# Kernel optimization log

Measured on AMD Instinct MI355X. Metric: run time of the kernel, lower is better.

The kernel has to match this reference:

```python
import jax, jax.numpy as jnp
import numpy as np

DIM = 512; NH = 8; HD = DIM // NH; WS = 28; N = WS * WS; H3 = (DIM * 4) // 3; EPS = 1e-6; B = 16


def _rel_pos_index(H, W):
    # static numpy computation of Swin-style relative position index [N, N]
    coords = np.stack(np.meshgrid(np.arange(H), np.arange(W), indexing='ij')).reshape(2, -1)
    rel = (coords[:, :, None] - coords[:, None, :]).transpose(1, 2, 0)
    rel[..., 0] += H - 1
    rel[..., 1] += W - 1
    rel[..., 0] *= 2 * W - 1
    return rel.sum(-1)

RPI = jnp.asarray(_rel_pos_index(WS, WS))  # [N, N] int


def adaptive_ln(x, w, b, a1w, a1b, a2w, a2b):
    # x: [B,C,H,W]; adapt params from global-avg-pooled 1x1 convs (== matmuls)
    C = x.shape[1]
    pooled = x.mean(axis=(2, 3))                      # [B,C]
    h = jax.nn.relu(pooled @ a1w.T + a1b)             # [B,C/4]
    ad = h @ a2w.T + a2b                              # [B,2C]
    aw = ad[:, :C][:, :, None, None]
    ab = ad[:, C:][:, :, None, None]
    u = x.mean(axis=1, keepdims=True)
    s = ((x - u) ** 2).mean(axis=1, keepdims=True)
    xn = (x - u) * jax.lax.rsqrt(s + EPS)
    return (w[None, :, None, None] * (1.0 + aw)) * xn + (b[None, :, None, None] + ab)


def dwconv(x, w, b):
    y = jax.lax.conv_general_dilated(x, w, (1, 1), 'SAME', feature_group_count=x.shape[1],
                                     dimension_numbers=('NCHW', 'OIHW', 'NCHW'))
    return y + b[None, :, None, None]


def conv1x1(x, w, b):
    return jnp.einsum('bchw,oc->bohw', x, w) + b[None, :, None, None]


def _forward(x, face_priors, n1_w, n1_b, n1_a1w, n1_a1b, n1_a2w, n1_a2b,
             n2_w, n2_b, n2_a1w, n2_a1b, n2_a2w, n2_a2b,
             qkv_w, qkv_b, rpb_table, struct_prior, proj_w, proj_b,
             eye_w, eye_b, nose_w, nose_b, mouth_w, mouth_b,
             fusion_w, fusion_b, gate1_w, gate1_b, gate2_w, gate2_b,
             es1_w, es1_b, es2_w, es2_b, em1_w, em1_b, em2_w, em2_b,
             el1_w, el1_b, el2_w, el2_b, router_w, router_b):
    Bx, C, H, W = x.shape
    n = H * W
    shortcut = x
    xa = adaptive_ln(x, n1_w, n1_b, n1_a1w, n1_a1b, n1_a2w, n1_a2b)
    # --- TripletFaceAttention ---
    xf = xa.reshape(Bx, C, n).transpose(0, 2, 1)                     # [B,N,C]
    qkv = (xf @ qkv_w.T + qkv_b).reshape(Bx, n, 3, NH, HD).transpose(2, 0, 3, 1, 4)
    q, k, v = qkv[0], qkv[1], qkv[2]                                 # [B,h,N,d]
    attn = jnp.einsum('bhnd,bhmd->bhnm', q, k) * (HD ** -0.5)
    attn = attn + struct_prior                                       # learned structure prior [1,h,N,N]
    rpb = rpb_table[RPI]                                             # [N,N,h]
    attn = attn + jnp.transpose(rpb, (2, 0, 1))[None]                # + relative position bias
    attn = attn * face_priors[:, None]                               # multiplicative face mask
    attn = jax.nn.softmax(attn, axis=-1)
    o = jnp.einsum('bhnm,bhmd->bhnd', attn, v).transpose(0, 2, 1, 3).reshape(Bx, n, C)
    o = o @ proj_w.T + proj_b
    x = shortcut + o.transpose(0, 2, 1).reshape(Bx, C, H, W)
    # --- FaceTokenMixer ---
    xn2 = adaptive_ln(x, n2_w, n2_b, n2_a1w, n2_a1b, n2_a2w, n2_a2b)
    cat = jnp.concatenate([dwconv(xn2, eye_w, eye_b),
                           dwconv(xn2, nose_w, nose_b),
                           dwconv(xn2, mouth_w, mouth_b)], axis=1)   # [B,3C,H,W]
    g = jax.nn.sigmoid(conv1x1(jax.nn.relu(conv1x1(xn2, gate1_w, gate1_b)), gate2_w, gate2_b))
    x = x + conv1x1(cat * g, fusion_w, fusion_b)
    # --- EfficientMLP (3-expert MoE, soft routing) ---
    r = jax.nn.softmax(x.mean(axis=(2, 3)) @ router_w.T + router_b, axis=-1)  # [B,3]
    def expert(w1, b1, w2, b2):
        return conv1x1(jax.nn.gelu(conv1x1(x, w1, b1), approximate=False), w2, b2)
    out = (r[:, 0, None, None, None] * expert(es1_w, es1_b, es2_w, es2_b)
           + r[:, 1, None, None, None] * expert(em1_w, em1_b, em2_w, em2_b)
           + r[:, 2, None, None, None] * expert(el1_w, el1_b, el2_w, el2_b))
    return x + out


def setup_inputs() -> dict:
    ks = iter(jax.random.split(jax.random.key(0), 64))
    def rn(shape, s=0.02):
        return jax.random.normal(next(ks), shape, jnp.float32) * s
    d = {}
    d['x'] = jax.random.normal(next(ks), (B, DIM, WS, WS), jnp.float32)
    d['face_priors'] = jax.random.uniform(next(ks), (B, N, N), jnp.float32)
    for p in ('n1', 'n2'):
        d[p + '_w'] = jnp.ones((DIM,), jnp.float32)
        d[p + '_b'] = jnp.zeros((DIM,), jnp.float32)
        d[p + '_a1w'] = rn((DIM // 4, DIM)); d[p + '_a1b'] = jnp.zeros((DIM // 4,), jnp.float32)
        d[p + '_a2w'] = rn((2 * DIM, DIM // 4)); d[p + '_a2b'] = jnp.zeros((2 * DIM,), jnp.float32)
    d['qkv_w'] = rn((3 * DIM, DIM)); d['qkv_b'] = jnp.zeros((3 * DIM,), jnp.float32)
    d['rpb_table'] = rn(((2 * WS - 1) ** 2, NH))
    d['struct_prior'] = rn((1, NH, N, N))
    d['proj_w'] = rn((DIM, DIM)); d['proj_b'] = jnp.zeros((DIM,), jnp.float32)
    d['eye_w'] = rn((DIM, 1, 3, 3)); d['eye_b'] = jnp.zeros((DIM,), jnp.float32)
    d['nose_w'] = rn((DIM, 1, 5, 5)); d['nose_b'] = jnp.zeros((DIM,), jnp.float32)
    d['mouth_w'] = rn((DIM, 1, 7, 7)); d['mouth_b'] = jnp.zeros((DIM,), jnp.float32)
    d['fusion_w'] = rn((DIM, 3 * DIM)); d['fusion_b'] = jnp.zeros((DIM,), jnp.float32)
    d['gate1_w'] = rn((DIM // 4, DIM)); d['gate1_b'] = jnp.zeros((DIM // 4,), jnp.float32)
    d['gate2_w'] = rn((3 * DIM, DIM // 4)); d['gate2_b'] = jnp.zeros((3 * DIM,), jnp.float32)
    for e in ('es', 'em', 'el'):
        d[e + '1_w'] = rn((H3, DIM)); d[e + '1_b'] = jnp.zeros((H3,), jnp.float32)
        d[e + '2_w'] = rn((DIM, H3)); d[e + '2_b'] = jnp.zeros((DIM,), jnp.float32)
    d['router_w'] = rn((3, DIM)); d['router_b'] = jnp.zeros((3,), jnp.float32)
    return d


def reference(x, face_priors, n1_w, n1_b, n1_a1w, n1_a1b, n1_a2w, n1_a2b,
              n2_w, n2_b, n2_a1w, n2_a1b, n2_a2w, n2_a2b,
              qkv_w, qkv_b, rpb_table, struct_prior, proj_w, proj_b,
              eye_w, eye_b, nose_w, nose_b, mouth_w, mouth_b,
              fusion_w, fusion_b, gate1_w, gate1_b, gate2_w, gate2_b,
              es1_w, es1_b, es2_w, es2_b, em1_w, em1_b, em2_w, em2_b,
              el1_w, el1_b, el2_w, el2_b, router_w, router_b):
    return _forward(x, face_priors, n1_w, n1_b, n1_a1w, n1_a1b, n1_a2w, n1_a2b,
                    n2_w, n2_b, n2_a1w, n2_a1b, n2_a2w, n2_a2b,
                    qkv_w, qkv_b, rpb_table, struct_prior, proj_w, proj_b,
                    eye_w, eye_b, nose_w, nose_b, mouth_w, mouth_b,
                    fusion_w, fusion_b, gate1_w, gate1_b, gate2_w, gate2_b,
                    es1_w, es1_b, es2_w, es2_b, em1_w, em1_b, em2_w, em2_b,
                    el1_w, el1_b, el2_w, el2_b, router_w, router_b)
```

## Files before the change

### kernel.cpp

```cpp
#include <hip/hip_runtime.h>
#include <math.h>


#define NPIX 784
#define CDIM 512
#define NHEAD 8
#define C3 1536

typedef unsigned int uint;
typedef unsigned short ushort;
typedef float f32x4 __attribute__((ext_vector_type(4)));
typedef __bf16 bf16x8 __attribute__((ext_vector_type(8)));
typedef __bf16 bf16x2 __attribute__((ext_vector_type(2)));

#define LOG2E 1.4426950408889634f
#define KSCL  0.18033688011112042f

#define OFF_XPM ((size_t)0)
#define OFF_W   ((size_t)3211264)
#define OFF_R2  ((size_t)5324288)
#define OFF_VBF ((size_t)14958080)
#define OFF_OBF ((size_t)18169344)
#define OFF_X2  ((size_t)21380608)
#define OFF_X3  ((size_t)27803136)
#define OFF_PL  ((size_t)34225664)
#define OFF_AD  ((size_t)34233856)
#define OFF_RB  ((size_t)34250240)
#define OFF_US  ((size_t)34250288)
#define OFF_RS  ((size_t)34262832)
#define OFF_E2C ((size_t)34275392)

#define WOFF_QKV 0
#define WOFF_PROJ 786432
#define WOFF_G1  1048576
#define WOFF_G2  1114112
#define WOFF_FUS 1310720
#define WOFF_E1  2097152

__device__ __forceinline__ ushort f2bf(float f) {
  __bf16 h = (__bf16)f;
  return __builtin_bit_cast(ushort, h);
}
__device__ __forceinline__ unsigned pack2bf(float lo, float hi) {
  bf16x2 v = {(__bf16)lo, (__bf16)hi};
  return __builtin_bit_cast(unsigned, v);
}
__device__ __forceinline__ float bf2f(ushort u) {
  unsigned x = ((unsigned)u) << 16;
  return __builtin_bit_cast(float, x);
}
__device__ __forceinline__ void unpack4bf(uint2 v, float* o) {
  o[0] = bf2f((ushort)(v.x & 0xffffu)); o[1] = bf2f((ushort)(v.x >> 16));
  o[2] = bf2f((ushort)(v.y & 0xffffu)); o[3] = bf2f((ushort)(v.y >> 16));
}

__global__ __launch_bounds__(64) void pool_mean_k(const float* __restrict__ x,
                                                  float* __restrict__ pooled) {
  int c = blockIdx.x, b = blockIdx.y;
  const float* row = x + ((size_t)b * CDIM + c) * NPIX;
  float s = 0.f;
  for (int i = threadIdx.x; i < NPIX; i += 64) s += row[i];
  #pragma unroll
  for (int off = 32; off; off >>= 1) s += __shfl_down(s, off);
  if (threadIdx.x == 0) pooled[b * CDIM + c] = s;
}

__global__ __launch_bounds__(256) void adapt_mlp_k(const float* __restrict__ pooled,
                                                   const float* __restrict__ a1w,
                                                   const float* __restrict__ a1b,
                                                   const float* __restrict__ a2w,
                                                   const float* __restrict__ a2b,
                                                   float* __restrict__ ad) {
  int b = blockIdx.x, tid = threadIdx.x;
  __shared__ float pl[CDIM];
  __shared__ float hh[128];
  for (int i = tid; i < CDIM; i += 256)
    pl[i] = pooled[b * CDIM + i] * (1.f / NPIX);
  __syncthreads();
  if (tid < 128) {
    const float* w = a1w + (size_t)tid * CDIM;
    float a = a1b[tid];
    for (int k = 0; k < CDIM; ++k) a += w[k] * pl[k];
    hh[tid] = fmaxf(a, 0.f);
  }
  __syncthreads();
  for (int o = tid; o < 1024; o += 256) {
    const float* w = a2w + (size_t)o * 128;
    float a = a2b[o];
    for (int k = 0; k < 128; ++k) a += w[k] * hh[k];
    ad[b * 1024 + o] = a;
  }
}

template <int STATS>
__global__ __launch_bounds__(256) void ln_pm_k(const float* __restrict__ x,
                                               const float* __restrict__ w,
                                               const float* __restrict__ bias,
                                               const float* __restrict__ ad,
                                               ushort* __restrict__ out,
                                               float* __restrict__ ust,
                                               float* __restrict__ rstp) {
  int b = blockIdx.y;
  int p0 = blockIdx.x * 32;
  int tid = threadIdx.x;
  int px = tid & 31, cg = tid >> 5;
  int p = p0 + px;
  bool valid = p < NPIX;
  const float* xb = x + (size_t)b * CDIM * NPIX;
  float s = 0.f, s2 = 0.f;
  if (valid) {
    for (int c = cg * 64; c < cg * 64 + 64; ++c) {
      float v = xb[(size_t)c * NPIX + p];
      s += v; s2 += v * v;
    }
  }
  __shared__ float rs[8][32], rq[8][32], us[32], vs[32];
  rs[cg][px] = s; rq[cg][px] = s2;
  __syncthreads();
  if (tid < 32) {
    float ts = 0.f, ts2 = 0.f;
    #pragma unroll
    for (int g = 0; g < 8; ++g) { ts += rs[g][tid]; ts2 += rq[g][tid]; }
    float u = ts * (1.f / CDIM);
    float var = ts2 * (1.f / CDIM) - u * u;
    float rv = rsqrtf(var + 1e-6f);
    us[tid] = u; vs[tid] = rv;
    if (STATS && p0 + tid < NPIX) {
      ust[(size_t)b * NPIX + p0 + tid] = u;
      rstp[(size_t)b * NPIX + p0 + tid] = rv;
    }
  }
  __syncthreads();
  if (valid) {
    float u = us[px], rv = vs[px];
    const float* aw = ad + (size_t)b * 1024;
    const float* ab = aw + CDIM;
    ushort* ob = out + ((size_t)(b * NPIX + p)) * CDIM + cg * 64;
    for (int cb = 0; cb < 64; cb += 8) {
      int c = cg * 64 + cb;
      float vv[8];
      #pragma unroll
      for (int q = 0; q < 8; ++q) {
        float v = xb[(size_t)(c + q) * NPIX + p];
        vv[q] = w[c + q] * (1.f + aw[c + q]) * ((v - u) * rv) + (bias[c + q] + ab[c + q]);
      }
      uint4 o = {pack2bf(vv[0], vv[1]), pack2bf(vv[2], vv[3]),
                 pack2bf(vv[4], vv[5]), pack2bf(vv[6], vv[7])};
      *(uint4*)(ob + cb) = o;
    }
  }
}

struct CvtDesc {
  const float* s[11];
  ushort* d[11];
  int rows[11], sk[11], dk[11], ds[11], rr[11];
};
__global__ __launch_bounds__(256) void cvt_w_k(CvtDesc D) {
  int seg = blockIdx.y;
  int sk = D.sk[seg], dk = D.dk[seg], ds = D.ds[seg], rr = D.rr[seg];
  int total = D.rows[seg] * dk;
  const float* s = D.s[seg];
  ushort* d = D.d[seg];
  for (int i = blockIdx.x * 256 + threadIdx.x; i < total; i += gridDim.x * 256) {
    int r = i / dk, cc = i - r * dk;
    d[(size_t)r * ds + cc] = (cc < sk && r < rr) ? f2bf(s[(size_t)r * sk + cc]) : (ushort)0;
  }
}

__global__ __launch_bounds__(256) void sprpb_k(const float* __restrict__ sp,
                                               const float* __restrict__ rpb,
                                               ushort* __restrict__ out) {
  const int q = blockIdx.x, h = blockIdx.y;
  const int i1 = q / 28, j1 = q - i1 * 28;
  const float* src = sp + ((size_t)h * NPIX + q) * NPIX;
  ushort* dst = out + ((size_t)h * NPIX + q) * NPIX;
  for (int m = threadIdx.x; m < NPIX; m += 256) {
    int i2 = m / 28, j2 = m - i2 * 28;
    float rv = rpb[(size_t)((i1 - i2 + 27) * 55 + (j1 - j2 + 27)) * NHEAD + h];
    dst[m] = f2bf((src[m] + rv) * LOG2E);
  }
}

__global__ __launch_bounds__(256) void fpcvt_k(const float* __restrict__ fp,
                                               ushort* __restrict__ out) {
  size_t i = (size_t)blockIdx.x * 256 + threadIdx.x;
  float4 v = *((const float4*)fp + i);
  ushort4 o;
  o.x = f2bf(v.x); o.y = f2bf(v.y); o.z = f2bf(v.z); o.w = f2bf(v.w);
  *((ushort4*)out + i) = o;
}

__global__ __launch_bounds__(512) void biaseff_k(const float* __restrict__ rbuf,
                                                 const float* __restrict__ b0,
                                                 const float* __restrict__ b1,
                                                 const float* __restrict__ b2,
                                                 const float* __restrict__ a0,
                                                 const float* __restrict__ a1,
                                                 const float* __restrict__ a2,
                                                 float* __restrict__ be,
                                                 float* __restrict__ e1bcat) {
  int b = blockIdx.x;
  if (b < 16) {
    int n = threadIdx.x;
    be[b * 512 + n] = rbuf[b * 3] * b0[n] + rbuf[b * 3 + 1] * b1[n] + rbuf[b * 3 + 2] * b2[n];
  } else {
    for (int i = threadIdx.x; i < 2112; i += 512) {
      int e = i / 704, r = i - e * 704;
      e1bcat[i] = (r < 682) ? (e == 0 ? a0 : e == 1 ? a1 : a2)[r] : 0.f;
    }
  }
}

template <int ORIENT, int EPI, int POOL, int DUALBF, int BN>
__global__ __launch_bounds__(256) void mgemm_k(const ushort* __restrict__ X,
                                               const ushort* __restrict__ Wt,
                                               const float* __restrict__ bias,
                                               const float* __restrict__ resid,
                                               const float* __restrict__ scales,
                                               void* __restrict__ OutV,
                                               float* __restrict__ pool_out,
                                               ushort* __restrict__ pm_out,
                                               int Ks, int Nreal, int Nstore) {
  constexpr int NFRAG = BN / 64;
  const int bid = blockIdx.x;
  const int xcd = bid & 7;
  const int i = bid >> 3;
  const int mt_local = i % 14;
  const int nt = i / 14;
  const int m0 = (xcd * 14 + mt_local) * 112;
  const int n0 = nt * BN;
  const int bb = m0 / NPIX;
  const int t = threadIdx.x;
  const int w = t >> 6, lane = t & 63, c = lane & 15, g = lane >> 4;
  __shared__ ushort Xs[7168];
  __shared__ ushort Ws[BN * 64];
  f32x4 acc[7][NFRAG];
  #pragma unroll
  for (int mi = 0; mi < 7; ++mi)
    #pragma unroll
    for (int ni = 0; ni < NFRAG; ++ni) acc[mi][ni] = (f32x4){0.f, 0.f, 0.f, 0.f};

  for (int k0 = 0; k0 < Ks; k0 += 64) {
    for (int ii = t; ii < 896; ii += 256) {
      int m = ii >> 3, kg = ii & 7;
      uint4 v = *(const uint4*)(X + (size_t)(m0 + m) * Ks + k0 + kg * 8);
      *(uint4*)&Xs[m * 64 + ((kg ^ (m & 7)) << 3)] = v;
    }
    for (int ii = t; ii < BN * 8; ii += 256) {
      int n = ii >> 3, kg = ii & 7;
      uint4 v = {0u, 0u, 0u, 0u};
      if (n0 + n < Nreal) v = *(const uint4*)(Wt + (size_t)(n0 + n) * Ks + k0 + kg * 8);
      *(uint4*)&Ws[n * 64 + ((kg ^ (n & 7)) << 3)] = v;
    }
    __syncthreads();
    #pragma unroll
    for (int kc = 0; kc < 2; ++kc) {
      bf16x8 xf[7], wf[NFRAG];
      #pragma unroll
      for (int mi = 0; mi < 7; ++mi) {
        int m = mi * 16 + c;
        xf[mi] = *(const bf16x8*)&Xs[m * 64 + (((kc * 4 + g) ^ (m & 7)) << 3)];
      }
      #pragma unroll
      for (int ni = 0; ni < NFRAG; ++ni) {
        int n = w * (16 * NFRAG) + ni * 16 + c;
        wf[ni] = *(const bf16x8*)&Ws[n * 64 + (((kc * 4 + g) ^ (n & 7)) << 3)];
      }
      #pragma unroll
      for (int mi = 0; mi < 7; ++mi)
        #pragma unroll
        for (int ni = 0; ni < NFRAG; ++ni)
          acc[mi][ni] = (ORIENT == 0)
            ? __builtin_amdgcn_mfma_f32_16x16x32_bf16(wf[ni], xf[mi], acc[mi][ni], 0, 0, 0)
            : __builtin_amdgcn_mfma_f32_16x16x32_bf16(xf[mi], wf[ni], acc[mi][ni], 0, 0, 0);
    }
    __syncthreads();
  }

  if (ORIENT == 0) {
    ushort* Ob = (ushort*)OutV;
    const int nbq = n0 + w * (16 * NFRAG);
    float bi[NFRAG][4];
    #pragma unroll
    for (int ni = 0; ni < NFRAG; ++ni)
      #pragma unroll
      for (int j = 0; j < 4; ++j) {
        int n = nbq + ni * 16 + g * 4 + j;
        bi[ni][j] = (n < Nreal) ? bias[n] : 0.f;
      }
    #pragma unroll
    for (int mi = 0; mi < 7; ++mi) {
      int m = m0 + mi * 16 + c;
      #pragma unroll
      for (int ni = 0; ni < NFRAG; ++ni) {
        int nb = nbq + ni * 16 + g * 4;
        if (nb >= Nstore) continue;
        float v[4];
        #pragma unroll
        for (int j = 0; j < 4; ++j) v[j] = acc[mi][ni][j] + bi[ni][j];
        if (EPI == 1) {
          #pragma unroll
          for (int j = 0; j < 4; ++j) v[j] = fmaxf(v[j], 0.f);
        } else if (EPI == 2) {
          #pragma unroll
          for (int j = 0; j < 4; ++j)
            v[j] = 0.5f * v[j] * (1.f + erff(v[j] * 0.70710678118654752f));
        } else if (EPI == 3) {
          uint2 cm = *(const uint2*)&Ob[(size_t)m * Nstore + nb];
          float cf[4];
          unpack4bf(cm, cf);
          #pragma unroll
          for (int j = 0; j < 4; ++j)
            v[j] = (1.f / (1.f + __expf(-v[j]))) * cf[j];
        } else if (EPI == 5) {
          int e = nb / 704; e = (e > 2) ? 2 : e;
          float sc = scales[bb * 3 + e];
          #pragma unroll
          for (int j = 0; j < 4; ++j)
            v[j] = 0.5f * v[j] * (1.f + erff(v[j] * 0.70710678118654752f)) * sc;
        }
        uint2 o = {pack2bf(v[0], v[1]), pack2bf(v[2], v[3])};
        *(uint2*)&Ob[(size_t)m * Nstore + nb] = o;
      }
    }
  } else {
    const int prow = m0 - bb * NPIX;
    float* Ob = (float*)OutV + (size_t)bb * CDIM * NPIX;
    const float* Rb = resid + (size_t)bb * CDIM * NPIX;
    float sc = (EPI == 4 && scales) ? scales[bb * 3] : 1.f;
    #pragma unroll
    for (int ni = 0; ni < NFRAG; ++ni) {
      int n = n0 + w * (16 * NFRAG) + ni * 16 + c;
      float bv = (EPI == 5) ? bias[(size_t)bb * CDIM + n] : bias[n];
      float cs = 0.f;
      #pragma unroll
      for (int mi = 0; mi < 7; ++mi) {
        int p = prow + mi * 16 + g * 4;
        size_t off = (size_t)n * NPIX + p;
        float4 r = *(const float4*)&Rb[off];
        f32x4 a = acc[mi][ni];
        float4 o = {r.x + sc * (a[0] + bv), r.y + sc * (a[1] + bv),
                    r.z + sc * (a[2] + bv), r.w + sc * (a[3] + bv)};
        *(float4*)&Ob[off] = o;
        if (POOL) cs += o.x + o.y + o.z + o.w;
        if (DUALBF) {
          size_t mg = (size_t)(m0 + mi * 16 + g * 4);
          pm_out[mg * CDIM + n] = f2bf(o.x);
          pm_out[(mg + 1) * CDIM + n] = f2bf(o.y);
          pm_out[(mg + 2) * CDIM + n] = f2bf(o.z);
          pm_out[(mg + 3) * CDIM + n] = f2bf(o.w);
        }
      }
      if (POOL) {
        cs += __shfl_xor(cs, 16);
        cs += __shfl_xor(cs, 32);
        if (g == 0) atomicAdd(pool_out + (size_t)bb * CDIM + n, cs);
      }
    }
  }
}

__global__ __launch_bounds__(256) void vtr_k(const ushort* __restrict__ qkvbf,
                                             ushort* __restrict__ vbf) {
  const int p0 = blockIdx.x * 64, c0 = blockIdx.y * 64, b = blockIdx.z;
  __shared__ ushort T[64][72];
  for (int idx = threadIdx.x; idx < 512; idx += 256) {
    int pl = idx >> 3, cq = idx & 7;
    int p = p0 + pl;
    uint4 v = {0u, 0u, 0u, 0u};
    if (p < NPIX)
      v = *(const uint4*)(qkvbf + (size_t)(b * NPIX + p) * C3 + 1024 + c0 + cq * 8);
    *(uint4*)&T[pl][cq * 8] = v;
  }
  __syncthreads();
  for (int idx = threadIdx.x; idx < 512; idx += 256) {
    int cl = idx >> 3, pq = idx & 7;
    if (p0 + pq * 8 < NPIX) {
      ushort tmp[8];
      #pragma unroll
      for (int i = 0; i < 8; ++i) tmp[i] = T[pq * 8 + i][cl];
      *(uint4*)(vbf + ((size_t)(b * CDIM + c0 + cl)) * NPIX + p0 + pq * 8) =
          *(const uint4*)&tmp[0];
    }
  }
}

struct KFr { bf16x8 a0, a1, b0, b1; };
struct VFr { bf16x8 v0, v1, v2, v3; };
struct BFr { uint2 sl, fl, sh, fh; };

__global__ __launch_bounds__(256) void attn_mfma_k(const ushort* __restrict__ qkvbf,
                                                   const ushort* __restrict__ vbf,
                                                   const ushort* __restrict__ sprpb,
                                                   const ushort* __restrict__ fpb,
                                                   ushort* __restrict__ obf) {
  const int bid = blockIdx.x;
  const int xcd = bid & 7;
  const int i = bid >> 3;
  const int b = xcd + 8 * (i / 56);
  const int r = i % 56;
  const int h = r & 7;
  const int qt = r >> 3;
  const int w = threadIdx.x >> 6, lane = threadIdx.x & 63;
  const int g = lane >> 4, c = lane & 15;
  const int q0 = qt * 128 + w * 32;
  if (q0 >= NPIX) return;
  const bool hasB = (q0 + 16) < NPIX;
  const int qA = q0 + c;
  const int qB = q0 + 16 + c;

  __shared__ uint BL[4][2][384];
  uint* bwA = BL[w][0];
  uint* bwB = BL[w][1];

  const ushort* qpA = qkvbf + (size_t)(b * NPIX + qA) * C3 + h * 64 + g * 8;
  const bf16x8 qfA0 = *(const bf16x8*)qpA;
  const bf16x8 qfA1 = *(const bf16x8*)(qpA + 32);
  bf16x8 qfB0 = qfA0, qfB1 = qfA1;
  if (hasB) {
    const ushort* qpB = qkvbf + (size_t)(b * NPIX + qB) * C3 + h * 64 + g * 8;
    qfB0 = *(const bf16x8*)qpB;
    qfB1 = *(const bf16x8*)(qpB + 32);
  }

  const ushort* kbase = qkvbf + (size_t)b * NPIX * C3 + 512 + h * 64 + g * 8;
  const ushort* vbase = vbf + ((size_t)b * CDIM + h * 64) * NPIX;
  const ushort* sprA = sprpb + ((size_t)h * NPIX + qA) * NPIX;
  const ushort* sprB = sprpb + ((size_t)h * NPIX + (hasB ? qB : qA)) * NPIX;
  const ushort* fpA = fpb + ((size_t)b * NPIX + qA) * NPIX;
  const ushort* fpB = fpb + ((size_t)b * NPIX + (hasB ? qB : qA)) * NPIX;

  auto load_k = [&](int m0, bool tfull) -> KFr {
    KFr k;
    const ushort* kp = kbase + (size_t)(m0 + c) * C3;
    k.a0 = *(const bf16x8*)kp;
    k.a1 = *(const bf16x8*)(kp + 32);
    const ushort* kp1 = kp + (tfull ? (size_t)16 * C3 : 0);
    k.b0 = *(const bf16x8*)kp1;
    k.b1 = *(const bf16x8*)(kp1 + 32);
    return k;
  };
  auto load_v = [&](int m0) -> VFr {
    VFr v;
    const ushort* vp = vbase + (size_t)c * NPIX + m0 + g * 8;
    v.v0 = *(const bf16x8*)(vp);
    v.v1 = *(const bf16x8*)(vp + (size_t)16 * NPIX);
    v.v2 = *(const bf16x8*)(vp + (size_t)32 * NPIX);
    v.v3 = *(const bf16x8*)(vp + (size_t)48 * NPIX);
    return v;
  };
  auto load_b = [&](const ushort* spr, const ushort* fp, int m0) -> BFr {
    BFr x;
    x.sl = *(const uint2*)(spr + m0 + g * 4);
    x.fl = *(const uint2*)(fp + m0 + g * 4);
    x.sh = *(const uint2*)(spr + m0 + 16 + g * 4);
    x.fh = *(const uint2*)(fp + m0 + 16 + g * 4);
    return x;
  };

  f32x4 oA0 = {0.f, 0.f, 0.f, 0.f}, oA1 = oA0, oA2 = oA0, oA3 = oA0;
  f32x4 oB0 = oA0, oB1 = oA0, oB2 = oA0, oB3 = oA0;
  float MA = -1e30f, LA = 0.f, MB = -1e30f, LB = 0.f;

  KFr kc = load_k(0, true);
  VFr vc = load_v(0);
  BFr bcA = load_b(sprA, fpA, 0);
  BFr bcB = bcA;
  if (hasB) bcB = load_b(sprB, fpB, 0);

  for (int ms = 0; ms < 25; ++ms) {
    const int m0 = ms * 32;
    const bool full = (ms < 24);

    KFr kn; VFr vn; BFr bnA, bnB;
    if (full) {
      const int nm0 = m0 + 32;
      kn = load_k(nm0, ms + 1 < 24);
      vn = load_v(nm0);
      bnA = load_b(sprA, fpA, nm0);
      if (hasB) bnB = load_b(sprB, fpB, nm0);
    }

    f32x4 sA0 = {0.f, 0.f, 0.f, 0.f}, sA1 = sA0;
    __builtin_amdgcn_s_setprio(1);
    sA0 = __builtin_amdgcn_mfma_f32_16x16x32_bf16(kc.a0, qfA0, sA0, 0, 0, 0);
    sA0 = __builtin_amdgcn_mfma_f32_16x16x32_bf16(kc.a1, qfA1, sA0, 0, 0, 0);
    if (full) {
      sA1 = __builtin_amdgcn_mfma_f32_16x16x32_bf16(kc.b0, qfA0, sA1, 0, 0, 0);
      sA1 = __builtin_amdgcn_mfma_f32_16x16x32_bf16(kc.b1, qfA1, sA1, 0, 0, 0);
    }
    __builtin_amdgcn_s_setprio(0);
    {
      float vA0[4], vA1[4];
      float spv[4], fpv[4];
      unpack4bf(bcA.sl, spv);
      unpack4bf(bcA.fl, fpv);
      #pragma unroll
      for (int j = 0; j < 4; ++j) vA0[j] = fmaf(sA0[j], KSCL, spv[j]) * fpv[j];
      if (full) {
        unpack4bf(bcA.sh, spv);
        unpack4bf(bcA.fh, fpv);
        #pragma unroll
        for (int j = 0; j < 4; ++j) vA1[j] = fmaf(sA1[j], KSCL, spv[j]) * fpv[j];
      }
      float tm = fmaxf(fmaxf(vA0[0], vA0[1]), fmaxf(vA0[2], vA0[3]));
      if (full) tm = fmaxf(tm, fmaxf(fmaxf(vA1[0], vA1[1]), fmaxf(vA1[2], vA1[3])));
      tm = fmaxf(tm, __shfl_xor(tm, 16));
      tm = fmaxf(tm, __shfl_xor(tm, 32));
      if (__any(tm > MA)) {
        const float nM = fmaxf(MA, tm);
        const float fac = __builtin_amdgcn_exp2f(MA - nM);
        LA *= fac;
        #pragma unroll
        for (int j = 0; j < 4; ++j) { oA0[j] *= fac; oA1[j] *= fac; oA2[j] *= fac; oA3[j] *= fac; }
        MA = nM;
      }
      float p0v[4], p1v[4];
      float ps = 0.f;
      #pragma unroll
      for (int j = 0; j < 4; ++j) { p0v[j] = __builtin_amdgcn_exp2f(vA0[j] - MA); ps += p0v[j]; }
      if (full) {
        #pragma unroll
        for (int j = 0; j < 4; ++j) { p1v[j] = __builtin_amdgcn_exp2f(vA1[j] - MA); ps += p1v[j]; }
      }
      ps += __shfl_xor(ps, 16);
      ps += __shfl_xor(ps, 32);
      LA += ps;
      uint2 wlo, whi;
      wlo.x = pack2bf(p0v[0], p0v[1]);
      wlo.y = pack2bf(p0v[2], p0v[3]);
      whi.x = full ? pack2bf(p1v[0], p1v[1]) : 0u;
      whi.y = full ? pack2bf(p1v[2], p1v[3]) : 0u;
      *(uint2*)&bwA[lane * 6] = wlo;
      *(uint2*)&bwA[lane * 6 + 2] = whi;
    }

    if (hasB) {
      f32x4 sB0 = {0.f, 0.f, 0.f, 0.f}, sB1 = sB0;
      __builtin_amdgcn_s_setprio(1);
      sB0 = __builtin_amdgcn_mfma_f32_16x16x32_bf16(kc.a0, qfB0, sB0, 0, 0, 0);
      sB0 = __builtin_amdgcn_mfma_f32_16x16x32_bf16(kc.a1, qfB1, sB0, 0, 0, 0);
      if (full) {
        sB1 = __builtin_amdgcn_mfma_f32_16x16x32_bf16(kc.b0, qfB0, sB1, 0, 0, 0);
        sB1 = __builtin_amdgcn_mfma_f32_16x16x32_bf16(kc.b1, qfB1, sB1, 0, 0, 0);
      }
      __builtin_amdgcn_s_setprio(0);
      float vB0[4], vB1[4];
      float spv[4], fpv[4];
      unpack4bf(bcB.sl, spv);
      unpack4bf(bcB.fl, fpv);
      #pragma unroll
      for (int j = 0; j < 4; ++j) vB0[j] = fmaf(sB0[j], KSCL, spv[j]) * fpv[j];
      if (full) {
        unpack4bf(bcB.sh, spv);
        unpack4bf(bcB.fh, fpv);
        #pragma unroll
        for (int j = 0; j < 4; ++j) vB1[j] = fmaf(sB1[j], KSCL, spv[j]) * fpv[j];
      }
      float tm = fmaxf(fmaxf(vB0[0], vB0[1]), fmaxf(vB0[2], vB0[3]));
      if (full) tm = fmaxf(tm, fmaxf(fmaxf(vB1[0], vB1[1]), fmaxf(vB1[2], vB1[3])));
      tm = fmaxf(tm, __shfl_xor(tm, 16));
      tm = fmaxf(tm, __shfl_xor(tm, 32));
      if (__any(tm > MB)) {
        const float nM = fmaxf(MB, tm);
        const float fac = __builtin_amdgcn_exp2f(MB - nM);
        LB *= fac;
        #pragma unroll
        for (int j = 0; j < 4; ++j) { oB0[j] *= fac; oB1[j] *= fac; oB2[j] *= fac; oB3[j] *= fac; }
        MB = nM;
      }
      float p0v[4], p1v[4];
      float ps = 0.f;
      #pragma unroll
      for (int j = 0; j < 4; ++j) { p0v[j] = __builtin_amdgcn_exp2f(vB0[j] - MB); ps += p0v[j]; }
      if (full) {
        #pragma unroll
        for (int j = 0; j < 4; ++j) { p1v[j] = __builtin_amdgcn_exp2f(vB1[j] - MB); ps += p1v[j]; }
      }
      ps += __shfl_xor(ps, 16);
      ps += __shfl_xor(ps, 32);
      LB += ps;
      uint2 wlo, whi;
      wlo.x = pack2bf(p0v[0], p0v[1]);
      wlo.y = pack2bf(p0v[2], p0v[3]);
      whi.x = full ? pack2bf(p1v[0], p1v[1]) : 0u;
      whi.y = full ? pack2bf(p1v[2], p1v[3]) : 0u;
      *(uint2*)&bwB[lane * 6] = wlo;
      *(uint2*)&bwB[lane * 6 + 2] = whi;
    }

    const int f = g >> 1;
    const int slo = 32 * (g & 1) + c;
    uint2 blo = *(const uint2*)&bwA[slo * 6 + f * 2];
    uint2 bhi = *(const uint2*)&bwA[(slo + 16) * 6 + f * 2];
    uint4 bba = {blo.x, blo.y, bhi.x, bhi.y};
    const bf16x8 pfA = __builtin_bit_cast(bf16x8, bba);
    __builtin_amdgcn_s_setprio(1);
    oA0 = __builtin_amdgcn_mfma_f32_16x16x32_bf16(vc.v0, pfA, oA0, 0, 0, 0);
    oA1 = __builtin_amdgcn_mfma_f32_16x16x32_bf16(vc.v1, pfA, oA1, 0, 0, 0);
    oA2 = __builtin_amdgcn_mfma_f32_16x16x32_bf16(vc.v2, pfA, oA2, 0, 0, 0);
    oA3 = __builtin_amdgcn_mfma_f32_16x16x32_bf16(vc.v3, pfA, oA3, 0, 0, 0);
    __builtin_amdgcn_s_setprio(0);
    if (hasB) {
      uint2 clo = *(const uint2*)&bwB[slo * 6 + f * 2];
      uint2 chi = *(const uint2*)&bwB[(slo + 16) * 6 + f * 2];
      uint4 bbb = {clo.x, clo.y, chi.x, chi.y};
      const bf16x8 pfB = __builtin_bit_cast(bf16x8, bbb);
      __builtin_amdgcn_s_setprio(1);
      oB0 = __builtin_amdgcn_mfma_f32_16x16x32_bf16(vc.v0, pfB, oB0, 0, 0, 0);
      oB1 = __builtin_amdgcn_mfma_f32_16x16x32_bf16(vc.v1, pfB, oB1, 0, 0, 0);
      oB2 = __builtin_amdgcn_mfma_f32_16x16x32_bf16(vc.v2, pfB, oB2, 0, 0, 0);
      oB3 = __builtin_amdgcn_mfma_f32_16x16x32_bf16(vc.v3, pfB, oB3, 0, 0, 0);
      __builtin_amdgcn_s_setprio(0);
    }

    if (full) { kc = kn; vc = vn; bcA = bnA; if (hasB) bcB = bnB; }
  }

  {
    const float invL = 1.f / LA;
    ushort* dst = obf + (size_t)(b * NPIX + qA) * CDIM + h * 64 + g * 4;
    f32x4 ot[4] = {oA0, oA1, oA2, oA3};
    #pragma unroll
    for (int t2 = 0; t2 < 4; ++t2) {
      uint2 o = {pack2bf(ot[t2][0] * invL, ot[t2][1] * invL),
                 pack2bf(ot[t2][2] * invL, ot[t2][3] * invL)};
      *(uint2*)(dst + t2 * 16) = o;
    }
  }
  if (hasB) {
    const float invL = 1.f / LB;
    ushort* dst = obf + (size_t)(b * NPIX + qB) * CDIM + h * 64 + g * 4;
    f32x4 ot[4] = {oB0, oB1, oB2, oB3};
    #pragma unroll
    for (int t2 = 0; t2 < 4; ++t2) {
      uint2 o = {pack2bf(ot[t2][0] * invL, ot[t2][1] * invL),
                 pack2bf(ot[t2][2] * invL, ot[t2][3] * invL)};
      *(uint2*)(dst + t2 * 16) = o;
    }
  }
}

__device__ __forceinline__ float bf2f_s(ushort u) { return bf2f(u); }

template <int R>
__device__ __forceinline__ void conv_pass(const ushort* __restrict__ plane_ci,
                                          const float* __restrict__ wl_ci,
                                          float bv, int slot,
                                          ushort (*__restrict__ outb)[16], int ci) {
  constexpr int K = 2 * R + 1;
  float wreg[K * K];
  #pragma unroll
  for (int i = 0; i < K * K; ++i) wreg[i] = wl_ci[i];
  #pragma unroll
  for (int r7 = 0; r7 < 7; ++r7) {
    const int run = slot + r7 * 16;
    const int y = run >> 2, x0 = (run & 3) * 7;
    float acc[7];
    #pragma unroll
    for (int i = 0; i < 7; ++i) acc[i] = bv;
    #pragma unroll
    for (int dy = 0; dy < K; ++dy) {
      const ushort* rp = plane_ci + (y + 3 - R + dy) * 34 + (x0 + 3 - R);
      float win[7 + 2 * R];
      #pragma unroll
      for (int k = 0; k < 7 + 2 * R; ++k) win[k] = bf2f_s(rp[k]);
      #pragma unroll
      for (int i = 0; i < 7; ++i)
        #pragma unroll
        for (int k = 0; k < K; ++k)
          acc[i] = fmaf(win[i + k], wreg[dy * K + k], acc[i]);
    }
    #pragma unroll
    for (int i = 0; i < 7; ++i) outb[y * 28 + x0 + i][ci] = f2bf(acc[i]);
  }
}

__global__ __launch_bounds__(256) void dwln_k(const float* __restrict__ x2,
    const float* __restrict__ ust, const float* __restrict__ rst,
    const float* __restrict__ ad, const float* __restrict__ n2w,
    const float* __restrict__ n2b,
    const float* __restrict__ ew, const float* __restrict__ eb,
    const float* __restrict__ nw, const float* __restrict__ nb,
    const float* __restrict__ mw, const float* __restrict__ mb,
    ushort* __restrict__ cat) {
  const int cg = blockIdx.x, b = blockIdx.y;
  const int c0 = cg * 16;
  const int t = threadIdx.x;
  const int ci = t & 15, slot = t >> 4;

  __shared__ ushort plane[16][1156];
  __shared__ ushort outb[784][16];
  __shared__ float Wl[16 * 49];
  __shared__ float LWs[16], LBs[16];

  {
    uint* pz = (uint*)&plane[0][0];
    for (int i = t; i < 16 * 1156 / 2; i += 256) pz[i] = 0u;
  }
  if (t < 16) {
    int cc = c0 + t;
    float aw = ad[b * 1024 + cc], ab = ad[b * 1024 + 512 + cc];
    LWs[t] = n2w[cc] * (1.f + aw);
    LBs[t] = n2b[cc] + ab;
  }
  __syncthreads();

  {
    float uu[4], rr[4];
    #pragma unroll
    for (int j = 0; j < 4; ++j) {
      int p = t + j * 256;
      if (p < NPIX) {
        uu[j] = ust[(size_t)b * NPIX + p];
        rr[j] = rst[(size_t)b * NPIX + p];
      }
    }
    for (int cc = 0; cc < 16; ++cc) {
      const float* xp = x2 + ((size_t)(b * CDIM + c0 + cc)) * NPIX;
      float lw = LWs[cc], lb = LBs[cc];
      #pragma unroll
      for (int j = 0; j < 4; ++j) {
        int p = t + j * 256;
        if (p < NPIX) {
          int y = p / 28, xx2 = p - y * 28;
          plane[cc][(y + 3) * 34 + xx2 + 3] = f2bf(lw * (xp[p] - uu[j]) * rr[j] + lb);
        }
      }
    }
  }
  __syncthreads();

  #pragma unroll 1
  for (int cv = 0; cv < 3; ++cv) {
    const float* gw = (cv == 0) ? ew : (cv == 1) ? nw : mw;
    const float* gb = (cv == 0) ? eb : (cv == 1) ? nb : mb;
    const int K2 = (cv == 0) ? 9 : (cv == 1) ? 25 : 49;
    for (int i = t; i < 16 * K2; i += 256) {
      int cc = i / K2, k = i - cc * K2;
      Wl[cc * K2 + k] = gw[(size_t)(c0 + cc) * K2 + k];
    }
    __syncthreads();
    float bv = gb[c0 + ci];
    if (cv == 0)      conv_pass<1>(&plane[ci][0], &Wl[ci * 9],  bv, slot, outb, ci);
    else if (cv == 1) conv_pass<2>(&plane[ci][0], &Wl[ci * 25], bv, slot, outb, ci);
    else              conv_pass<3>(&plane[ci][0], &Wl[ci * 49], bv, slot, outb, ci);
    __syncthreads();
    for (int idx = t; idx < NPIX * 2; idx += 256) {
      int p = idx >> 1, half = idx & 1;
      uint4 v = *(const uint4*)&outb[p][half * 8];
      *(uint4*)(cat + ((size_t)(b * NPIX + p)) * C3 + cv * 512 + c0 + half * 8) = v;
    }
    __syncthreads();
  }
}

__global__ __launch_bounds__(64) void router_k(const float* __restrict__ pooled,
                                               const float* __restrict__ rw,
                                               const float* __restrict__ rb,
                                               float* __restrict__ r) {
  int b = blockIdx.x, lane = threadIdx.x;
  float a0 = 0.f, a1 = 0.f, a2 = 0.f;
  for (int k = lane; k < CDIM; k += 64) {
    float p = pooled[b * CDIM + k] * (1.f / NPIX);
    a0 += rw[k] * p;
    a1 += rw[CDIM + k] * p;
    a2 += rw[2 * CDIM + k] * p;
  }
  #pragma unroll
  for (int off = 32; off; off >>= 1) {
    a0 += __shfl_down(a0, off);
    a1 += __shfl_down(a1, off);
    a2 += __shfl_down(a2, off);
  }
  if (lane == 0) {
    float l0 = a0 + rb[0], l1 = a1 + rb[1], l2 = a2 + rb[2];
    float mx = fmaxf(l0, fmaxf(l1, l2));
    float e0 = __expf(l0 - mx), e1 = __expf(l1 - mx), e2 = __expf(l2 - mx);
    float inv = 1.f / (e0 + e1 + e2);
    r[b * 3 + 0] = e0 * inv;
    r[b * 3 + 1] = e1 * inv;
    r[b * 3 + 2] = e2 * inv;
  }
}

extern "C" void kernel_launch(void* const* d_in, const int* in_sizes, int n_in,
                              void* d_out, int out_size, void* d_ws, size_t ws_size,
                              hipStream_t stream) {
  (void)in_sizes; (void)n_in; (void)out_size; (void)ws_size;
  const float* x         = (const float*)d_in[0];
  const float* fpri      = (const float*)d_in[1];
  const float* n1_w      = (const float*)d_in[2];
  const float* n1_b      = (const float*)d_in[3];
  const float* n1_a1w    = (const float*)d_in[4];
  const float* n1_a1b    = (const float*)d_in[5];
  const float* n1_a2w    = (const float*)d_in[6];
  const float* n1_a2b    = (const float*)d_in[7];
  const float* n2_w      = (const float*)d_in[8];
  const float* n2_b      = (const float*)d_in[9];
  const float* n2_a1w    = (const float*)d_in[10];
  const float* n2_a1b    = (const float*)d_in[11];
  const float* n2_a2w    = (const float*)d_in[12];
  const float* n2_a2b    = (const float*)d_in[13];
  const float* qkv_w     = (const float*)d_in[14];
  const float* qkv_b     = (const float*)d_in[15];
  const float* rpb_table = (const float*)d_in[16];
  const float* sprior    = (const float*)d_in[17];
  const float* proj_w    = (const float*)d_in[18];
  const float* proj_b    = (const float*)d_in[19];
  const float* eye_w     = (const float*)d_in[20];
  const float* eye_b     = (const float*)d_in[21];
  const float* nose_w    = (const float*)d_in[22];
  const float* nose_b    = (const float*)d_in[23];
  const float* mouth_w   = (const float*)d_in[24];
  const float* mouth_b   = (const float*)d_in[25];
  const float* fusion_w  = (const float*)d_in[26];
  const float* fusion_b  = (const float*)d_in[27];
  const float* gate1_w   = (const float*)d_in[28];
  const float* gate1_b   = (const float*)d_in[29];
  const float* gate2_w   = (const float*)d_in[30];
  const float* gate2_b   = (const float*)d_in[31];
  const float* e1w[3] = {(const float*)d_in[32], (const float*)d_in[36], (const float*)d_in[40]};
  const float* e1b[3] = {(const float*)d_in[33], (const float*)d_in[37], (const float*)d_in[41]};
  const float* e2w[3] = {(const float*)d_in[34], (const float*)d_in[38], (const float*)d_in[42]};
  const float* e2b[3] = {(const float*)d_in[35], (const float*)d_in[39], (const float*)d_in[43]};
  const float* router_w  = (const float*)d_in[44];
  const float* router_b  = (const float*)d_in[45];

  float* ws    = (float*)d_ws;
  ushort* xpm  = (ushort*)(ws + OFF_XPM);
  ushort* wb   = (ushort*)(ws + OFF_W);
  ushort* r2u  = (ushort*)(ws + OFF_R2);
  ushort* vbf  = (ushort*)(ws + OFF_VBF);
  ushort* obf  = (ushort*)(ws + OFF_OBF);
  float* x2    = ws + OFF_X2;
  float* x3    = ws + OFF_X3;
  float* pld   = ws + OFF_PL;
  float* adb   = ws + OFF_AD;
  float* rbuf  = ws + OFF_RB;
  float* ust   = ws + OFF_US;
  float* rst   = ws + OFF_RS;
  float* outp  = (float*)d_out;

  ushort* qkvw  = wb + WOFF_QKV;
  ushort* projw = wb + WOFF_PROJ;
  ushort* g1w   = wb + WOFF_G1;
  ushort* g2w   = wb + WOFF_G2;
  ushort* fusw  = wb + WOFF_FUS;
  ushort* e1cat = wb + WOFF_E1;
  ushort* e2cat = (ushort*)(ws + OFF_E2C);
  float* be     = adb;
  float* e1bcat = adb + 8192;

  ushort* fpbf   = (ushort*)x2;
  ushort* sprpbf = (ushort*)x3;

  CvtDesc D;
  auto seg = [&](int s2, const float* src, ushort* dst, int rows, int sk, int dk,
                 int ds, int rr) {
    D.s[s2] = src; D.d[s2] = dst; D.rows[s2] = rows; D.sk[s2] = sk;
    D.dk[s2] = dk; D.ds[s2] = ds; D.rr[s2] = rr;
  };
  seg(0, qkv_w,    qkvw,  1536, 512,  512,  512,  1536);
  seg(1, proj_w,   projw, 512,  512,  512,  512,  512);
  seg(2, gate1_w,  g1w,   128,  512,  512,  512,  128);
  seg(3, gate2_w,  g2w,   1536, 128,  128,  128,  1536);
  seg(4, fusion_w, fusw,  512,  1536, 1536, 1536, 512);
  for (int e = 0; e < 3; ++e) {
    seg(5 + e, e1w[e], e1cat + (size_t)e * 704 * 512, 704, 512, 512, 512, 682);
    seg(8 + e, e2w[e], e2cat + (size_t)e * 704,       512, 682, 704, 2112, 512);
  }
  cvt_w_k<<<dim3(512, 11), 256, 0, stream>>>(D);

  sprpb_k<<<dim3(NPIX, NHEAD), 256, 0, stream>>>(sprior, rpb_table, sprpbf);
  fpcvt_k<<<9604, 256, 0, stream>>>(fpri, fpbf);

  pool_mean_k<<<dim3(CDIM, 16), 64, 0, stream>>>(x, pld);
  adapt_mlp_k<<<16, 256, 0, stream>>>(pld, n1_a1w, n1_a1b, n1_a2w, n1_a2b, adb);
  ln_pm_k<0><<<dim3(25, 16), 256, 0, stream>>>(x, n1_w, n1_b, adb, xpm, nullptr, nullptr);

  mgemm_k<0, 0, 0, 0, 128><<<1344, 256, 0, stream>>>(xpm, qkvw, qkv_b, nullptr, nullptr,
                                                     r2u, nullptr, nullptr, 512, 1536, 1536);
  vtr_k<<<dim3(13, 8, 16), 256, 0, stream>>>(r2u, vbf);
  attn_mfma_k<<<896, 256, 0, stream>>>(r2u, vbf, sprpbf, fpbf, obf);
  hipMemsetAsync(pld, 0, 16 * CDIM * sizeof(float), stream);
  mgemm_k<1, 4, 1, 0, 64><<<896, 256, 0, stream>>>(obf, projw, proj_b, x, nullptr,
                                                   x2, pld, nullptr, 512, 512, 512);

  adapt_mlp_k<<<16, 256, 0, stream>>>(pld, n2_a1w, n2_a1b, n2_a2w, n2_a2b, adb);
  ln_pm_k<1><<<dim3(25, 16), 256, 0, stream>>>(x2, n2_w, n2_b, adb, xpm, ust, rst);
  dwln_k<<<dim3(32, 16), 256, 0, stream>>>(x2, ust, rst, adb, n2_w, n2_b,
                                           eye_w, eye_b, nose_w, nose_b, mouth_w, mouth_b,
                                           r2u);
  mgemm_k<0, 1, 0, 0, 64><<<224, 256, 0, stream>>>(xpm, g1w, gate1_b, nullptr, nullptr,
                                                   obf, nullptr, nullptr, 512, 128, 128);
  mgemm_k<0, 3, 0, 0, 128><<<1344, 256, 0, stream>>>(obf, g2w, gate2_b, nullptr, nullptr,
                                                     r2u, nullptr, nullptr, 128, 1536, 1536);
  hipMemsetAsync(pld, 0, 16 * CDIM * sizeof(float), stream);
  mgemm_k<1, 4, 1, 1, 64><<<896, 256, 0, stream>>>(r2u, fusw, fusion_b, x2, nullptr,
                                                   x3, pld, xpm, 1536, 512, 512);

  router_k<<<16, 64, 0, stream>>>(pld, router_w, router_b, rbuf);
  biaseff_k<<<17, 512, 0, stream>>>(rbuf, e2b[0], e2b[1], e2b[2],
                                    e1b[0], e1b[1], e1b[2], be, e1bcat);
  mgemm_k<0, 5, 0, 0, 128><<<1904, 256, 0, stream>>>(xpm, e1cat, e1bcat, nullptr, rbuf,
                                                     r2u, nullptr, nullptr, 512, 2112, 2112);
  mgemm_k<1, 5, 0, 0, 64><<<896, 256, 0, stream>>>(r2u, e2cat, be, x3, nullptr,
                                                   outp, nullptr, nullptr, 2112, 512, 512);
}
```

Measured before the change: 724.7 us.

## Fuse V transpose into QKV GEMM epilogue and deepen bias prefetch in attention

```diff
diff --git a/kernel.cpp b/kernel.cpp
--- a/kernel.cpp
+++ b/kernel.cpp
@@ -212,7 +212,7 @@
   }
 }
 
-template <int ORIENT, int EPI, int POOL, int DUALBF, int BN>
+template <int ORIENT, int EPI, int POOL, int DUALBF, int DUALV, int BN>
 __global__ __launch_bounds__(256) void mgemm_k(const ushort* __restrict__ X,
                                                const ushort* __restrict__ Wt,
                                                const float* __restrict__ bias,
@@ -322,6 +322,12 @@
         }
         uint2 o = {pack2bf(v[0], v[1]), pack2bf(v[2], v[3])};
         *(uint2*)&Ob[(size_t)m * Nstore + nb] = o;
+        if (DUALV && nb >= 1024) {
+          const int p = m - bb * NPIX;
+          #pragma unroll
+          for (int j = 0; j < 4; ++j)
+            pm_out[((size_t)bb * CDIM + (nb + j - 1024)) * NPIX + p] = f2bf(v[j]);
+        }
       }
     }
   } else {
@@ -357,31 +363,6 @@
         cs += __shfl_xor(cs, 32);
         if (g == 0) atomicAdd(pool_out + (size_t)bb * CDIM + n, cs);
       }
-    }
-  }
-}
-
-__global__ __launch_bounds__(256) void vtr_k(const ushort* __restrict__ qkvbf,
-                                             ushort* __restrict__ vbf) {
-  const int p0 = blockIdx.x * 64, c0 = blockIdx.y * 64, b = blockIdx.z;
-  __shared__ ushort T[64][72];
-  for (int idx = threadIdx.x; idx < 512; idx += 256) {
-    int pl = idx >> 3, cq = idx & 7;
-    int p = p0 + pl;
-    uint4 v = {0u, 0u, 0u, 0u};
-    if (p < NPIX)
-      v = *(const uint4*)(qkvbf + (size_t)(b * NPIX + p) * C3 + 1024 + c0 + cq * 8);
-    *(uint4*)&T[pl][cq * 8] = v;
-  }
-  __syncthreads();
-  for (int idx = threadIdx.x; idx < 512; idx += 256) {
-    int cl = idx >> 3, pq = idx & 7;
-    if (p0 + pq * 8 < NPIX) {
-      ushort tmp[8];
-      #pragma unroll
-      for (int i = 0; i < 8; ++i) tmp[i] = T[pq * 8 + i][cl];
-      *(uint4*)(vbf + ((size_t)(b * CDIM + c0 + cl)) * NPIX + p0 + pq * 8) =
-          *(const uint4*)&tmp[0];
     }
   }
 }
@@ -466,20 +447,29 @@
   KFr kc = load_k(0, true);
   VFr vc = load_v(0);
   BFr bcA = load_b(sprA, fpA, 0);
-  BFr bcB = bcA;
-  if (hasB) bcB = load_b(sprB, fpB, 0);
+  BFr bnA = load_b(sprA, fpA, 32);
+  BFr bcB = bcA, bnB = bnA;
+  if (hasB) {
+    bcB = load_b(sprB, fpB, 0);
+    bnB = load_b(sprB, fpB, 32);
+  }
 
   for (int ms = 0; ms < 25; ++ms) {
     const int m0 = ms * 32;
     const bool full = (ms < 24);
 
-    KFr kn; VFr vn; BFr bnA, bnB;
+    KFr kn; VFr vn; BFr b2A, b2B;
     if (full) {
       const int nm0 = m0 + 32;
       kn = load_k(nm0, ms + 1 < 24);
       vn = load_v(nm0);
-      bnA = load_b(sprA, fpA, nm0);
-      if (hasB) bnB = load_b(sprB, fpB, nm0);
+      if (ms + 2 <= 24) {
+        b2A = load_b(sprA, fpA, m0 + 64);
+        if (hasB) b2B = load_b(sprB, fpB, m0 + 64);
+      } else {
+        b2A = bnA;
+        if (hasB) b2B = bnB;
+      }
     }
 
     f32x4 sA0 = {0.f, 0.f, 0.f, 0.f}, sA1 = sA0;
@@ -615,7 +605,11 @@
       __builtin_amdgcn_s_setprio(0);
     }
 
-    if (full) { kc = kn; vc = vn; bcA = bnA; if (hasB) bcB = bnB; }
+    if (full) {
+      kc = kn; vc = vn;
+      bcA = bnA; bnA = b2A;
+      if (hasB) { bcB = bnB; bnB = b2B; }
+    }
   }
 
   {
@@ -880,32 +874,31 @@
   adapt_mlp_k<<<16, 256, 0, stream>>>(pld, n1_a1w, n1_a1b, n1_a2w, n1_a2b, adb);
   ln_pm_k<0><<<dim3(25, 16), 256, 0, stream>>>(x, n1_w, n1_b, adb, xpm, nullptr, nullptr);
 
-  mgemm_k<0, 0, 0, 0, 128><<<1344, 256, 0, stream>>>(xpm, qkvw, qkv_b, nullptr, nullptr,
-                                                     r2u, nullptr, nullptr, 512, 1536, 1536);
-  vtr_k<<<dim3(13, 8, 16), 256, 0, stream>>>(r2u, vbf);
+  mgemm_k<0, 0, 0, 0, 1, 128><<<1344, 256, 0, stream>>>(xpm, qkvw, qkv_b, nullptr, nullptr,
+                                                        r2u, nullptr, vbf, 512, 1536, 1536);
   attn_mfma_k<<<896, 256, 0, stream>>>(r2u, vbf, sprpbf, fpbf, obf);
   hipMemsetAsync(pld, 0, 16 * CDIM * sizeof(float), stream);
-  mgemm_k<1, 4, 1, 0, 64><<<896, 256, 0, stream>>>(obf, projw, proj_b, x, nullptr,
-                                                   x2, pld, nullptr, 512, 512, 512);
+  mgemm_k<1, 4, 1, 0, 0, 64><<<896, 256, 0, stream>>>(obf, projw, proj_b, x, nullptr,
+                                                      x2, pld, nullptr, 512, 512, 512);
 
   adapt_mlp_k<<<16, 256, 0, stream>>>(pld, n2_a1w, n2_a1b, n2_a2w, n2_a2b, adb);
   ln_pm_k<1><<<dim3(25, 16), 256, 0, stream>>>(x2, n2_w, n2_b, adb, xpm, ust, rst);
   dwln_k<<<dim3(32, 16), 256, 0, stream>>>(x2, ust, rst, adb, n2_w, n2_b,
                                            eye_w, eye_b, nose_w, nose_b, mouth_w, mouth_b,
                                            r2u);
-  mgemm_k<0, 1, 0, 0, 64><<<224, 256, 0, stream>>>(xpm, g1w, gate1_b, nullptr, nullptr,
-                                                   obf, nullptr, nullptr, 512, 128, 128);
-  mgemm_k<0, 3, 0, 0, 128><<<1344, 256, 0, stream>>>(obf, g2w, gate2_b, nullptr, nullptr,
-                                                     r2u, nullptr, nullptr, 128, 1536, 1536);
+  mgemm_k<0, 1, 0, 0, 0, 64><<<224, 256, 0, stream>>>(xpm, g1w, gate1_b, nullptr, nullptr,
+                                                      obf, nullptr, nullptr, 512, 128, 128);
+  mgemm_k<0, 3, 0, 0, 0, 128><<<1344, 256, 0, stream>>>(obf, g2w, gate2_b, nullptr, nullptr,
+                                                        r2u, nullptr, nullptr, 128, 1536, 1536);
   hipMemsetAsync(pld, 0, 16 * CDIM * sizeof(float), stream);
-  mgemm_k<1, 4, 1, 1, 64><<<896, 256, 0, stream>>>(r2u, fusw, fusion_b, x2, nullptr,
-                                                   x3, pld, xpm, 1536, 512, 512);
+  mgemm_k<1, 4, 1, 1, 0, 64><<<896, 256, 0, stream>>>(r2u, fusw, fusion_b, x2, nullptr,
+                                                      x3, pld, xpm, 1536, 512, 512);
 
   router_k<<<16, 64, 0, stream>>>(pld, router_w, router_b, rbuf);
   biaseff_k<<<17, 512, 0, stream>>>(rbuf, e2b[0], e2b[1], e2b[2],
                                     e1b[0], e1b[1], e1b[2], be, e1bcat);
-  mgemm_k<0, 5, 0, 0, 128><<<1904, 256, 0, stream>>>(xpm, e1cat, e1bcat, nullptr, rbuf,
-                                                     r2u, nullptr, nullptr, 512, 2112, 2112);
-  mgemm_k<1, 5, 0, 0, 64><<<896, 256, 0, stream>>>(r2u, e2cat, be, x3, nullptr,
-                                                   outp, nullptr, nullptr, 2112, 512, 512);
-}
+  mgemm_k<0, 5, 0, 0, 0, 128><<<1904, 256, 0, stream>>>(xpm, e1cat, e1bcat, nullptr, rbuf,
+                                                        r2u, nullptr, nullptr, 512, 2112, 2112);
+  mgemm_k<1, 5, 0, 0, 0, 64><<<896, 256, 0, stream>>>(r2u, e2cat, be, x3, nullptr,
+                                                      outp, nullptr, nullptr, 2112, 512, 512);
+}
```

After: 723.3 us. Within noise of the previous version (-0.2%).
